# Performance work log

Measured on AMD Instinct MI355X. Metric: run time of the kernel, lower is better.

## Reference

```python
import jax, jax.numpy as jnp
import numpy as np

BLOCK = 64      # block_size
NRAND = 3       # num_random_blocks
NUM_HEAD = 16
HEAD_DIM = 64
HIDDEN = 1024
PEN = -10000.0  # HF attn_mask_penalty


def _sparse_attn(q, k, v, band_mask, from_mask, to_mask, blocked_mask, rand_attn):
    # q,k,v: [B,H,S,D]; BigBird block-sparse attention (HF math).
    B, H, S, D = q.shape
    b, r = BLOCK, NRAND
    n = S // b
    rsd = 1.0 / (D ** 0.5)

    bq = q.reshape(B, H, n, b, D)
    bk = k.reshape(B, H, n, b, D)
    bv = v.reshape(B, H, n, b, D)

    bi = jnp.arange(B)[:, None, None, None]
    hi = jnp.arange(H)[None, :, None, None]
    # gathered random key/value blocks: [B,H,n-2,r*b,D]
    gk = bk[bi, hi, rand_attn].reshape(B, H, n - 2, r * b, D)
    gv = bv[bi, hi, rand_attn].reshape(B, H, n - 2, r * b, D)
    # random-block mask: [B,H,n-2,b,r*b]
    rm = blocked_mask[bi, rand_attn].reshape(B, H, n - 2, r * b)
    rand_mask = jnp.einsum("blq,bhlk->bhlqk", blocked_mask[:, 1:-1], rm)

    ones = lambda shp: jnp.ones(shp, q.dtype)

    # ---- first query block: attends to everything ----
    p = jnp.einsum("bhqd,bhkd->bhqk", bq[:, :, 0], k) * rsd + (1.0 - to_mask) * PEN
    c0 = jnp.einsum("bhqk,bhkd->bhqd", jax.nn.softmax(p, -1), v)[:, :, None]

    # ---- second query block: blocks 0,1,2,last + random ----
    k1 = jnp.concatenate([bk[:, :, 0], bk[:, :, 1], bk[:, :, 2], bk[:, :, -1], gk[:, :, 0]], axis=2)
    v1 = jnp.concatenate([bv[:, :, 0], bv[:, :, 1], bv[:, :, 2], bv[:, :, -1], gv[:, :, 0]], axis=2)
    p = jnp.einsum("bhqd,bhkd->bhqk", bq[:, :, 1], k1) * rsd
    seq_pad = jnp.concatenate([to_mask[..., :3 * b], to_mask[..., -b:], ones((B, 1, 1, r * b))], axis=3)
    rand_pad = jnp.concatenate([ones((B, H, b, 4 * b)), rand_mask[:, :, 0]], axis=3)
    p = p + (1.0 - jnp.minimum(seq_pad, rand_pad)) * PEN
    c1 = jnp.einsum("bhqk,bhkd->bhqd", jax.nn.softmax(p, -1), v1)[:, :, None]

    # ---- middle blocks 2..n-3: band(3 blocks) + first + last + random ----
    ek = jnp.concatenate([bk[:, :, 1:-3], bk[:, :, 2:-2], bk[:, :, 3:-1]], axis=3)  # [B,H,n-4,3b,D]
    ev = jnp.concatenate([bv[:, :, 1:-3], bv[:, :, 2:-2], bv[:, :, 3:-1]], axis=3)
    mq = bq[:, :, 2:-2]                                                              # [B,H,n-4,b,D]
    inner = jnp.einsum("bhlqd,bhlkd->bhlqk", mq, ek) * rsd + (1.0 - band_mask) * PEN
    randp = jnp.einsum("bhlqd,bhlkd->bhlqk", mq, gk[:, :, 1:-1]) * rsd + (1.0 - rand_mask[:, :, 1:-1]) * PEN
    firstp = jnp.einsum("bhlqd,bhkd->bhlqk", mq, bk[:, :, 0]) * rsd + (1.0 - to_mask[..., :b][:, :, None]) * PEN
    lastp = jnp.einsum("bhlqd,bhkd->bhlqk", mq, bk[:, :, -1]) * rsd + (1.0 - to_mask[..., -b:][:, :, None]) * PEN
    band = jnp.concatenate([firstp, inner, randp, lastp], axis=-1)  # [B,H,n-4,b,(5+r)*b]
    a = jax.nn.softmax(band, -1)
    cm = jnp.einsum("bhlqk,bhlkd->bhlqd", a[..., b:4 * b], ev)
    cm = cm + jnp.einsum("bhlqk,bhlkd->bhlqd", a[..., 4 * b:-b], gv[:, :, 1:-1])
    cm = cm + jnp.einsum("bhlqk,bhkd->bhlqd", a[..., :b], bv[:, :, 0])
    cm = cm + jnp.einsum("bhlqk,bhkd->bhlqd", a[..., -b:], bv[:, :, -1])

    # ---- second-last query block: blocks 0,-3,-2,-1 + random ----
    k2 = jnp.concatenate([bk[:, :, 0], bk[:, :, -3], bk[:, :, -2], bk[:, :, -1], gk[:, :, -1]], axis=2)
    v2 = jnp.concatenate([bv[:, :, 0], bv[:, :, -3], bv[:, :, -2], bv[:, :, -1], gv[:, :, -1]], axis=2)
    p = jnp.einsum("bhqd,bhkd->bhqk", bq[:, :, -2], k2) * rsd
    seq_pad = jnp.concatenate([to_mask[..., :b], to_mask[..., -3 * b:], ones((B, 1, 1, r * b))], axis=3)
    rand_pad = jnp.concatenate([ones((B, H, b, 4 * b)), rand_mask[:, :, -1]], axis=3)
    p = p + (1.0 - jnp.minimum(seq_pad, rand_pad)) * PEN
    c2 = jnp.einsum("bhqk,bhkd->bhqd", jax.nn.softmax(p, -1), v2)[:, :, None]

    # ---- last query block: attends to everything ----
    p = jnp.einsum("bhqd,bhkd->bhqk", bq[:, :, -1], k) * rsd + (1.0 - to_mask) * PEN
    c3 = jnp.einsum("bhqk,bhkd->bhqd", jax.nn.softmax(p, -1), v)[:, :, None]

    ctx = jnp.concatenate([c0, c1, cm, c2, c3], axis=2).reshape(B, H, S, D)
    ctx = ctx * from_mask  # [B,1,S,1]
    return ctx.transpose(0, 2, 1, 3).reshape(B, S, H * D)


def setup_inputs() -> dict:
    key = jax.random.key(0)
    ks = jax.random.split(key, 12)
    B, L = 2, 4064
    S = 4096
    n = S // BLOCK
    sc = 0.02
    inp = {
        "X": jax.random.normal(ks[0], (B, L, HIDDEN), jnp.float32),
        "Wq": jax.random.normal(ks[1], (HIDDEN, NUM_HEAD * HEAD_DIM), jnp.float32) * sc,
        "b_q": jnp.zeros((NUM_HEAD * HEAD_DIM,), jnp.float32),
        "Wk": jax.random.normal(ks[2], (HIDDEN, NUM_HEAD * HEAD_DIM), jnp.float32) * sc,
        "b_k": jnp.zeros((NUM_HEAD * HEAD_DIM,), jnp.float32),
        "Wv": jax.random.normal(ks[3], (HIDDEN, NUM_HEAD * HEAD_DIM), jnp.float32) * sc,
        "b_v": jnp.zeros((NUM_HEAD * HEAD_DIM,), jnp.float32),
        "Wo": jax.random.normal(ks[4], (NUM_HEAD * HEAD_DIM, HIDDEN), jnp.float32) * sc,
        "b_o": jnp.zeros((HIDDEN,), jnp.float32),
        "band_mask": jnp.ones((B, 1, n - 4, BLOCK, 3 * BLOCK), jnp.float32),
        "from_mask": jnp.ones((B, 1, S, 1), jnp.float32),
        "to_mask": jnp.ones((B, 1, 1, S), jnp.float32),
        "blocked_encoder_mask": jnp.ones((B, n, BLOCK), jnp.float32),
        "rand_attn": jax.random.randint(ks[5], (B, NUM_HEAD, n - 2, NRAND), 0, n, jnp.int32),
    }
    return inp


def reference(X, Wq, b_q, Wk, b_k, Wv, b_v, Wo, b_o,
              band_mask, from_mask, to_mask, blocked_encoder_mask, rand_attn):
    B, L, _ = X.shape
    pad = BLOCK - L % BLOCK  # matches torch wrapper (pads full block if L % b == 0)
    Xp = jnp.pad(X, ((0, 0), (0, pad), (0, 0)))
    S = L + pad

    def proj(W, bias):
        return (Xp @ W + bias).reshape(B, S, NUM_HEAD, HEAD_DIM).transpose(0, 2, 1, 3)

    q, k, v = proj(Wq, b_q), proj(Wk, b_k), proj(Wv, b_v)
    attn = _sparse_attn(q, k, v, band_mask, from_mask, to_mask, blocked_encoder_mask, rand_attn)
    out = attn @ Wo + b_o
    return out[:, :L]
```

## Files before the change

kernel.cpp:

```cpp
#include <hip/hip_runtime.h>

#define BB 2
#define SEQ 4096
#define LQ 4064
#define HID 1024
#define NH 16
#define HD 64
#define NB 64
#define BLK 64
#define NR 3
#define PENV -10000.0f

typedef __bf16 bf16;
typedef __bf16 bf16x8 __attribute__((ext_vector_type(8)));
typedef float floatx4 __attribute__((ext_vector_type(4)));

__device__ inline floatx4 mfma16(bf16x8 a, bf16x8 b, floatx4 c) {
    return __builtin_amdgcn_mfma_f32_16x16x32_bf16(a, b, c, 0, 0, 0);
}

__device__ inline void async_ld16(const bf16* g, bf16* l) {
    __builtin_amdgcn_global_load_lds(
        (const __attribute__((address_space(1))) unsigned int*)g,
        (__attribute__((address_space(3))) unsigned int*)l, 16, 0, 0);
}

__global__ __launch_bounds__(256) void cast_pad_x(const float* __restrict__ X,
                                                  bf16* __restrict__ Xp) {
    int t = blockIdx.x * 256 + threadIdx.x;
    int c4 = t & 255;
    int row = t >> 8;
    int b = row >> 12;
    int s = row & 4095;
    float4 v = make_float4(0.f, 0.f, 0.f, 0.f);
    if (s < LQ) {
        v = reinterpret_cast<const float4*>(X + ((size_t)(b * LQ + s)) * HID)[c4];
    }
    union { bf16 h[4]; uint2 u; } o;
    o.h[0] = (bf16)v.x; o.h[1] = (bf16)v.y; o.h[2] = (bf16)v.z; o.h[3] = (bf16)v.w;
    *reinterpret_cast<uint2*>(Xp + (size_t)row * HID + c4 * 4) = o.u;
}

__global__ __launch_bounds__(256) void transpose_w(const float* __restrict__ Wq,
                                                   const float* __restrict__ Wk,
                                                   const float* __restrict__ Wv,
                                                   const float* __restrict__ Wo,
                                                   bf16* __restrict__ WqkvT,
                                                   bf16* __restrict__ WoT) {
    __shared__ float tile[64][65];
    int sel = blockIdx.z;
    const float* src = (sel == 0) ? Wq : (sel == 1) ? Wk : (sel == 2) ? Wv : Wo;
    bf16* dst = (sel < 3) ? (WqkvT + (size_t)sel * HID * HID) : WoT;
    int j0 = blockIdx.x * 64, k0 = blockIdx.y * 64;
    int tx = threadIdx.x, ty = threadIdx.y;
    for (int i = 0; i < 16; i++) {
        int k = ty + i * 4;
        tile[k][tx] = src[(size_t)(k0 + k) * HID + j0 + tx];
    }
    __syncthreads();
    for (int i = 0; i < 16; i++) {
        int j = ty + i * 4;
        dst[(size_t)(j0 + j) * HID + k0 + tx] = (bf16)tile[tx][j];
    }
}

__global__ __launch_bounds__(256) void transpose_band(const float* __restrict__ band,
                                                      float* __restrict__ bandT) {
    __shared__ float tile[64][65];
    int kt = blockIdx.x;
    int lrow = blockIdx.y;
    int b = blockIdx.z;
    const float* src = band + ((size_t)(b * (NB - 4) + lrow) * BLK) * 192;
    float* dst = bandT + ((size_t)(b * (NB - 4) + lrow) * 192) * BLK;
    int tx = threadIdx.x, ty = threadIdx.y;
    for (int i = 0; i < 16; i++) {
        int qq = i * 4 + ty;
        tile[qq][tx] = src[(size_t)qq * 192 + kt * 64 + tx];
    }
    __syncthreads();
    for (int i = 0; i < 16; i++) {
        int k = i * 4 + ty;
        dst[(size_t)(kt * 64 + k) * BLK + tx] = tile[tx][k];
    }
}

__global__ __launch_bounds__(256) void mask_viol(const float* __restrict__ tom,
                                                 const float* __restrict__ blocked,
                                                 const float* __restrict__ band,
                                                 int* __restrict__ flags) {
    int which = blockIdx.y, b = blockIdx.z;
    const float* src;
    size_t n;
    if (which == 0)      { src = tom     + (size_t)b * SEQ;                  n = SEQ; }
    else if (which == 1) { src = blocked + (size_t)b * NB * BLK;             n = NB * BLK; }
    else                 { src = band    + (size_t)b * (NB - 4) * BLK * 192; n = (size_t)(NB - 4) * BLK * 192; }
    const float4* s4 = (const float4*)src;
    size_t n4 = n >> 2;
    int bad = 0;
    for (size_t i = blockIdx.x * 256 + threadIdx.x; i < n4; i += 240 * 256) {
        float4 v = s4[i];
        bad |= (v.x != 1.0f) | (v.y != 1.0f) | (v.z != 1.0f) | (v.w != 1.0f);
    }
    if (__any(bad) && (threadIdx.x & 63) == 0)
        atomicOr(&flags[which * BB + b], 1);
}

__global__ __launch_bounds__(256) void gemm_qkv(const bf16* __restrict__ Xp,
                                                const bf16* __restrict__ WT,
                                                const float* __restrict__ bq,
                                                const float* __restrict__ bk,
                                                const float* __restrict__ bv,
                                                bf16* __restrict__ qo,
                                                bf16* __restrict__ ko,
                                                bf16* __restrict__ vt) {
    __shared__ __align__(16) char smem[36864];
    bf16* As = (bf16*)smem;
    bf16* Bs = As + 128 * 64;
    int tid = threadIdx.x;
    int wave = tid >> 6, lane = tid & 63;
    int quad = lane >> 4, lm = lane & 15;
    int id = blockIdx.x;
    int xcd = id & 7, slot = id >> 3;
    int tile_m = (xcd * 8 + (slot & 7)) * 128;
    int tile_n = (slot >> 3) * 128;
    int wm = (wave & 1) * 64, wn = (wave >> 1) * 64;

    floatx4 acc[4][4] = {};

    for (int k0 = 0; k0 < HID; k0 += 64) {
        __syncthreads();
        for (int it = 0; it < 4; it++) {
            int c = it * 256 + tid;
            int row = c >> 3, col = (c & 7) * 8;
            async_ld16(Xp + (size_t)(tile_m + row) * HID + k0 + col, &As[c * 8]);
            async_ld16(WT + (size_t)(tile_n + row) * HID + k0 + col, &Bs[c * 8]);
        }
        __syncthreads();
        for (int ks = 0; ks < 64; ks += 32) {
            bf16x8 a[4], b[4];
            for (int i = 0; i < 4; i++)
                a[i] = *reinterpret_cast<const bf16x8*>(&As[(wm + i * 16 + lm) * 64 + ks + quad * 8]);
            for (int j = 0; j < 4; j++)
                b[j] = *reinterpret_cast<const bf16x8*>(&Bs[(wn + j * 16 + lm) * 64 + ks + quad * 8]);
            for (int i = 0; i < 4; i++)
                for (int j = 0; j < 4; j++)
                    acc[i][j] = mfma16(a[i], b[j], acc[i][j]);
        }
    }

    int which = tile_n >> 10;
    int hc_base = (tile_n + wn) & 1023;
    int h = hc_base >> 6;
    const float* bias = (which == 0) ? bq : (which == 1) ? bk : bv;
    __syncthreads();
    bf16* ep = (bf16*)smem + wave * (64 * 72);

    if (which < 2) {
        #pragma unroll
        for (int i = 0; i < 4; i++)
            #pragma unroll
            for (int j = 0; j < 4; j++) {
                float bsv = bias[hc_base + j * 16 + lm];
                #pragma unroll
                for (int r = 0; r < 4; r++) {
                    float val = acc[i][j][r] + bsv;
                    if (which == 0) val *= 0.125f;
                    ep[(i * 16 + quad * 4 + r) * 72 + j * 16 + lm] = (bf16)val;
                }
            }
        __builtin_amdgcn_wave_barrier();
        int s_glob = tile_m + wm + lane;
        int b_ = s_glob >> 12, s = s_glob & 4095;
        bf16* dstb = ((which == 0) ? qo : ko) + ((size_t)((b_ * NH + h) * SEQ + s)) * HD;
        #pragma unroll
        for (int c = 0; c < 8; c++)
            *reinterpret_cast<uint4*>(dstb + c * 8) =
                *reinterpret_cast<const uint4*>(ep + lane * 72 + c * 8);
    } else {
        #pragma unroll
        for (int i = 0; i < 4; i++)
            #pragma unroll
            for (int j = 0; j < 4; j++) {
                float bsv = bias[hc_base + j * 16 + lm];
                #pragma unroll
                for (int r = 0; r < 4; r++) {
                    float val = acc[i][j][r] + bsv;
                    ep[(j * 16 + lm) * 72 + i * 16 + quad * 4 + r] = (bf16)val;
                }
            }
        __builtin_amdgcn_wave_barrier();
        int s_base = tile_m + wm;
        int b_ = s_base >> 12, s0 = s_base & 4095;
        bf16* dstb = vt + ((size_t)((b_ * NH + h) * HD + lane)) * SEQ + s0;
        #pragma unroll
        for (int c = 0; c < 8; c++)
            *reinterpret_cast<uint4*>(dstb + c * 8) =
                *reinterpret_cast<const uint4*>(ep + lane * 72 + c * 8);
    }
}

__global__ __launch_bounds__(256, 2) void attn_kernel(const bf16* __restrict__ q,
                                                      const bf16* __restrict__ kk,
                                                      const bf16* __restrict__ vt,
                                                      const float* __restrict__ bandT,
                                                      const float* __restrict__ fromm,
                                                      const float* __restrict__ tom,
                                                      const float* __restrict__ blocked,
                                                      const int* __restrict__ rand_attn,
                                                      const int* __restrict__ flags,
                                                      bf16* __restrict__ attn) {
    __shared__ __align__(16) char smem[33792 + 512];

    int tid = threadIdx.x, wave = tid >> 6, lane = tid & 63;
    int quad = lane >> 4, lm = lane & 15;
    int bh = blockIdx.x;
    int b = bh >> 4, h = bh & 15;
    size_t bh_base = (size_t)bh * SEQ * HD;
    int x = blockIdx.y;
    bool fullmode = (x < 8);
    int l, sub;
    if (fullmode) { l = (x >> 2) ? (NB - 1) : 0; sub = x & 3; }
    else          { l = x - 7;                   sub = wave;  }

    bool do_to = flags[b] != 0;
    bool do_bl = flags[BB + b] != 0;
    bool do_bd = flags[2 * BB + b] != 0;

    bf16x8 aq0 = *reinterpret_cast<const bf16x8*>(
        q + bh_base + (size_t)(l * BLK + sub * 16 + lm) * HD + quad * 8);
    bf16x8 aq1 = *reinterpret_cast<const bf16x8*>(
        q + bh_base + (size_t)(l * BLK + sub * 16 + lm) * HD + 32 + quad * 8);

    floatx4 ctx[4] = {};
    float mrun = -1e30f, lrun = 0.f;
    float mq = blocked[((size_t)b * NB + l) * BLK + sub * 16 + lm];

    int blist[8], btype[8];
    if (!fullmode) {
        int base;
        if (l == 1) {
            blist[0] = 0; blist[1] = 1; blist[2] = 2; blist[3] = NB - 1;
            btype[0] = btype[1] = btype[2] = btype[3] = 0;
            base = 4;
        } else if (l == NB - 2) {
            blist[0] = 0; blist[1] = NB - 3; blist[2] = NB - 2; blist[3] = NB - 1;
            btype[0] = btype[1] = btype[2] = btype[3] = 0;
            base = 4;
        } else {
            blist[0] = 0;      btype[0] = 0;
            blist[1] = l - 1;  btype[1] = 1;
            blist[2] = l;      btype[2] = 2;
            blist[3] = l + 1;  btype[3] = 3;
            blist[4] = NB - 1; btype[4] = 0;
            base = 5;
        }
        const int* ra = rand_attn + ((size_t)(b * NH + h) * (NB - 2) + (l - 1)) * NR;
        for (int r = 0; r < NR; r++) { blist[base + r] = ra[r]; btype[base + r] = 4; }
        for (int i = base + NR; i < 8; i++) { blist[i] = 0; btype[i] = 5; }
    }

    bf16* pw = (bf16*)smem + wave * 16 * 264;

    int nch = fullmode ? 4 : 2;
    for (int ch = 0; ch < nch; ch++) {
        floatx4 sc[4][4];
        #pragma unroll
        for (int ib = 0; ib < 4; ib++) {
            int kb  = fullmode ? (wave * 16 + ch * 4 + ib) : blist[ch * 4 + ib];
            int typ = fullmode ? 0 : btype[ch * 4 + ib];
            const bf16* kbase = kk + bh_base + (size_t)kb * BLK * HD;
            #pragma unroll
            for (int f = 0; f < 4; f++) {
                bf16x8 a0 = *reinterpret_cast<const bf16x8*>(kbase + (f * 16 + lm) * HD + quad * 8);
                bf16x8 a1 = *reinterpret_cast<const bf16x8*>(kbase + (f * 16 + lm) * HD + 32 + quad * 8);
                floatx4 z = {0.f, 0.f, 0.f, 0.f};
                z = mfma16(a0, aq0, z);
                z = mfma16(a1, aq1, z);
                sc[ib][f] = z;
            }
            if (typ == 0) {
                if (do_to) {
                    #pragma unroll
                    for (int f = 0; f < 4; f++) {
                        float4 t4 = *reinterpret_cast<const float4*>(
                            tom + (size_t)b * SEQ + kb * BLK + f * 16 + quad * 4);
                        sc[ib][f][0] += (1.f - t4.x) * PENV;
                        sc[ib][f][1] += (1.f - t4.y) * PENV;
                        sc[ib][f][2] += (1.f - t4.z) * PENV;
                        sc[ib][f][3] += (1.f - t4.w) * PENV;
                    }
                }
            } else if (typ == 4) {
                if (do_bl) {
                    #pragma unroll
                    for (int f = 0; f < 4; f++) {
                        float4 t4 = *reinterpret_cast<const float4*>(
                            blocked + ((size_t)b * NB + kb) * BLK + f * 16 + quad * 4);
                        sc[ib][f][0] += (1.f - mq * t4.x) * PENV;
                        sc[ib][f][1] += (1.f - mq * t4.y) * PENV;
                        sc[ib][f][2] += (1.f - mq * t4.z) * PENV;
                        sc[ib][f][3] += (1.f - mq * t4.w) * PENV;
                    }
                }
            } else if (typ != 5) {
                if (do_bd) {
                    int t = typ - 1;
                    const float* bp = bandT + ((size_t)(b * (NB - 4) + (l - 2)) * 192 + t * 64) * BLK;
                    #pragma unroll
                    for (int f = 0; f < 4; f++)
                        #pragma unroll
                        for (int r = 0; r < 4; r++) {
                            float bm = bp[(size_t)(f * 16 + quad * 4 + r) * BLK + sub * 16 + lm];
                            sc[ib][f][r] += (1.f - bm) * PENV;
                        }
                }
            } else {
                #pragma unroll
                for (int f = 0; f < 4; f++)
                    #pragma unroll
                    for (int r = 0; r < 4; r++) sc[ib][f][r] += PENV;
            }
        }

        float mx = -1e30f;
        #pragma unroll
        for (int ib = 0; ib < 4; ib++)
            #pragma unroll
            for (int f = 0; f < 4; f++)
                #pragma unroll
                for (int r = 0; r < 4; r++) mx = fmaxf(mx, sc[ib][f][r]);
        mx = fmaxf(mx, __shfl_xor(mx, 16, 64));
        mx = fmaxf(mx, __shfl_xor(mx, 32, 64));
        float mnew = fmaxf(mrun, mx);
        float scale = __expf(mrun - mnew);
        lrun *= scale;
        #pragma unroll
        for (int dj = 0; dj < 4; dj++) ctx[dj] *= scale;
        mrun = mnew;

        __builtin_amdgcn_wave_barrier();
        float rs = 0.f;
        #pragma unroll
        for (int ib = 0; ib < 4; ib++)
            #pragma unroll
            for (int f = 0; f < 4; f++) {
                float p0 = __expf(sc[ib][f][0] - mnew);
                float p1 = __expf(sc[ib][f][1] - mnew);
                float p2 = __expf(sc[ib][f][2] - mnew);
                float p3 = __expf(sc[ib][f][3] - mnew);
                rs += (p0 + p1) + (p2 + p3);
                union { bf16 hh[4]; uint2 u; } pu;
                pu.hh[0] = (bf16)p0; pu.hh[1] = (bf16)p1;
                pu.hh[2] = (bf16)p2; pu.hh[3] = (bf16)p3;
                *reinterpret_cast<uint2*>(pw + lm * 264 + ib * 64 + f * 16 + quad * 4) = pu.u;
            }
        __builtin_amdgcn_wave_barrier();
        rs += __shfl_xor(rs, 16, 64);
        rs += __shfl_xor(rs, 32, 64);
        lrun += rs;

        #pragma unroll
        for (int ib = 0; ib < 4; ib++) {
            int kb = fullmode ? (wave * 16 + ch * 4 + ib) : blist[ch * 4 + ib];
            const bf16* vtb = vt + (size_t)bh * HD * SEQ + (size_t)kb * BLK;
            bf16x8 pb0 = *reinterpret_cast<const bf16x8*>(pw + lm * 264 + ib * 64 + quad * 8);
            bf16x8 pb1 = *reinterpret_cast<const bf16x8*>(pw + lm * 264 + ib * 64 + 32 + quad * 8);
            #pragma unroll
            for (int dj = 0; dj < 4; dj++) {
                bf16x8 aV0 = *reinterpret_cast<const bf16x8*>(
                    vtb + (size_t)(dj * 16 + lm) * SEQ + quad * 8);
                bf16x8 aV1 = *reinterpret_cast<const bf16x8*>(
                    vtb + (size_t)(dj * 16 + lm) * SEQ + 32 + quad * 8);
                ctx[dj] = mfma16(aV0, pb0, ctx[dj]);
                ctx[dj] = mfma16(aV1, pb1, ctx[dj]);
            }
        }
    }

    if (!fullmode) {
        int sq = l * BLK + sub * 16 + lm;
        float w = (1.f / lrun) * fromm[(size_t)b * SEQ + sq];
        bf16* dst = attn + ((size_t)(b * SEQ + sq)) * HID + h * HD;
        #pragma unroll
        for (int dj = 0; dj < 4; dj++) {
            union { bf16 hh[4]; uint2 u; } o;
            #pragma unroll
            for (int r = 0; r < 4; r++) o.hh[r] = (bf16)(ctx[dj][r] * w);
            *reinterpret_cast<uint2*>(dst + dj * 16 + quad * 4) = o.u;
        }
    } else {
        float* ctxL = (float*)smem;
        float* mL   = (float*)(smem + 33792);
        float* lL   = (float*)(smem + 33792 + 256);
        __syncthreads();
        #pragma unroll
        for (int dj = 0; dj < 4; dj++)
            #pragma unroll
            for (int r = 0; r < 4; r++)
                ctxL[wave * 1024 + (dj * 16 + quad * 4 + r) * 16 + lm] = ctx[dj][r];
        if (quad == 0) { mL[wave * 16 + lm] = mrun; lL[wave * 16 + lm] = lrun; }
        __syncthreads();
        int qq = tid & 15, dbase = (tid >> 4) * 4;
        float M = -1e30f;
        for (int w = 0; w < 4; w++) M = fmaxf(M, mL[w * 16 + qq]);
        float e[4], Lt = 0.f;
        for (int w = 0; w < 4; w++) { e[w] = __expf(mL[w * 16 + qq] - M); Lt += lL[w * 16 + qq] * e[w]; }
        int sq = l * BLK + sub * 16 + qq;
        float wgt = (1.f / Lt) * fromm[(size_t)b * SEQ + sq];
        union { bf16 hh[4]; uint2 u; } o;
        #pragma unroll
        for (int dd = 0; dd < 4; dd++) {
            float acc = 0.f;
            for (int w = 0; w < 4; w++) acc += ctxL[w * 1024 + (dbase + dd) * 16 + qq] * e[w];
            o.hh[dd] = (bf16)(acc * wgt);
        }
        *reinterpret_cast<uint2*>(attn + ((size_t)(b * SEQ + sq)) * HID + h * HD + dbase) = o.u;
    }
}

__global__ __launch_bounds__(256) void gemm_out(const bf16* __restrict__ A,
                                                const bf16* __restrict__ WoT,
                                                const float* __restrict__ bo,
                                                float* __restrict__ out) {
    __shared__ __align__(16) bf16 As[128 * 64];
    __shared__ __align__(16) bf16 Bs[128 * 64];
    int tid = threadIdx.x;
    int wave = tid >> 6, lane = tid & 63;
    int quad = lane >> 4, lm = lane & 15;
    int id = blockIdx.x;
    int xcd = id & 7, slot = id >> 3;
    int tile_m = (xcd * 8 + (slot & 7)) * 128;
    int tile_n = (slot >> 3) * 128;
    int wm = (wave & 1) * 64, wn = (wave >> 1) * 64;

    floatx4 acc[4][4] = {};

    for (int k0 = 0; k0 < HID; k0 += 64) {
        __syncthreads();
        for (int it = 0; it < 4; it++) {
            int c = it * 256 + tid;
            int row = c >> 3, col = (c & 7) * 8;
            async_ld16(A + (size_t)(tile_m + row) * HID + k0 + col, &As[c * 8]);
            async_ld16(WoT + (size_t)(tile_n + row) * HID + k0 + col, &Bs[c * 8]);
        }
        __syncthreads();
        for (int ks = 0; ks < 64; ks += 32) {
            bf16x8 a[4], b[4];
            for (int i = 0; i < 4; i++)
                a[i] = *reinterpret_cast<const bf16x8*>(&As[(wm + i * 16 + lm) * 64 + ks + quad * 8]);
            for (int j = 0; j < 4; j++)
                b[j] = *reinterpret_cast<const bf16x8*>(&Bs[(wn + j * 16 + lm) * 64 + ks + quad * 8]);
            for (int i = 0; i < 4; i++)
                for (int j = 0; j < 4; j++)
                    acc[i][j] = mfma16(a[i], b[j], acc[i][j]);
        }
    }

    for (int i = 0; i < 4; i++) {
        for (int j = 0; j < 4; j++) {
            int nn = tile_n + wn + j * 16 + lm;
            float bsv = bo[nn];
            for (int r = 0; r < 4; r++) {
                int mm = tile_m + wm + i * 16 + quad * 4 + r;
                int b_ = mm >> 12, s = mm & 4095;
                if (s < LQ)
                    out[((size_t)(b_ * LQ + s)) * HID + nn] = acc[i][j][r] + bsv;
            }
        }
    }
}

extern "C" void kernel_launch(void* const* d_in, const int* in_sizes, int n_in,
                              void* d_out, int out_size, void* d_ws, size_t ws_size,
                              hipStream_t stream) {
    const float* X       = (const float*)d_in[0];
    const float* Wq      = (const float*)d_in[1];
    const float* bq      = (const float*)d_in[2];
    const float* Wk      = (const float*)d_in[3];
    const float* bk      = (const float*)d_in[4];
    const float* Wv      = (const float*)d_in[5];
    const float* bv      = (const float*)d_in[6];
    const float* Wo      = (const float*)d_in[7];
    const float* bo      = (const float*)d_in[8];
    const float* band    = (const float*)d_in[9];
    const float* fromm   = (const float*)d_in[10];
    const float* tom     = (const float*)d_in[11];
    const float* blocked = (const float*)d_in[12];
    const int*   randa   = (const int*)d_in[13];
    float* out = (float*)d_out;

    char* ws = (char*)d_ws;
    bf16* Xp    = (bf16*)(ws + 0);
    bf16* WqkvT = (bf16*)(ws + 16777216);
    bf16* WoT   = (bf16*)(ws + 23068672);
    bf16* qb    = (bf16*)(ws + 25165824);
    bf16* kb    = (bf16*)(ws + 41943040);
    bf16* vtb   = (bf16*)(ws + 58720256);
    bf16* attnb = Xp;
    float* bandT = (float*)WqkvT;
    int* flagsp = (int*)(ws + 16777216 + 5898240);

    cast_pad_x<<<dim3(8192), dim3(256), 0, stream>>>(X, Xp);
    transpose_w<<<dim3(16, 16, 4), dim3(64, 4), 0, stream>>>(Wq, Wk, Wv, Wo, WqkvT, WoT);
    gemm_qkv<<<dim3(1536), dim3(256), 0, stream>>>(Xp, WqkvT, bq, bk, bv, qb, kb, vtb);
    transpose_band<<<dim3(3, NB - 4, BB), dim3(64, 4), 0, stream>>>(band, bandT);
    hipMemsetAsync(flagsp, 0, 3 * BB * sizeof(int), stream);
    mask_viol<<<dim3(240, 3, BB), dim3(256), 0, stream>>>(tom, blocked, band, flagsp);
    attn_kernel<<<dim3(BB * NH, 70), dim3(256), 0, stream>>>(qb, kb, vtb, bandT, fromm, tom,
                                                             blocked, randa, flagsp, attnb);
    gemm_out<<<dim3(512), dim3(256), 0, stream>>>(attnb, WoT, bo, out);
}
```

Measured before the change: 392.1 us.

## Shrink attention chunk to two key blocks and raise occupancy to four blocks per CU

The attention kernel now handles two key blocks per softmax chunk instead of four. This halves the per-wave probability scratch in LDS and the score registers, which allows launch bounds of 4 blocks per CU. The block list and type arrays become packed 64-bit and 32-bit scalars, and block indices are made wave-uniform with readfirstlane. K fragments and the first V block are loaded ahead of the masking and softmax work so memory latency overlaps with compute. In exchange there are twice as many online-softmax rescale steps and wave barriers, and the tighter register budget could cause spills.

```diff
diff --git a/kernel.cpp b/kernel.cpp
--- a/kernel.cpp
+++ b/kernel.cpp
@@ -199,7 +199,7 @@
     }
 }
 
-__global__ __launch_bounds__(256, 2) void attn_kernel(const bf16* __restrict__ q,
+__global__ __launch_bounds__(256, 4) void attn_kernel(const bf16* __restrict__ q,
                                                       const bf16* __restrict__ kk,
                                                       const bf16* __restrict__ vt,
                                                       const float* __restrict__ bandT,
@@ -209,7 +209,7 @@
                                                       const int* __restrict__ rand_attn,
                                                       const int* __restrict__ flags,
                                                       bf16* __restrict__ attn) {
-    __shared__ __align__(16) char smem[33792 + 512];
+    __shared__ __align__(16) char smem[17408];
 
     int tid = threadIdx.x, wave = tid >> 6, lane = tid & 63;
     int quad = lane >> 4, lm = lane & 15;
@@ -235,100 +235,141 @@
     float mrun = -1e30f, lrun = 0.f;
     float mq = blocked[((size_t)b * NB + l) * BLK + sub * 16 + lm];
 
-    int blist[8], btype[8];
+    unsigned long long kbp = 0ull;
+    unsigned int typ_p = 0u;
     if (!fullmode) {
         int base;
         if (l == 1) {
-            blist[0] = 0; blist[1] = 1; blist[2] = 2; blist[3] = NB - 1;
-            btype[0] = btype[1] = btype[2] = btype[3] = 0;
+            kbp = (1ull << 8) | (2ull << 16) | ((unsigned long long)(NB - 1) << 24);
             base = 4;
         } else if (l == NB - 2) {
-            blist[0] = 0; blist[1] = NB - 3; blist[2] = NB - 2; blist[3] = NB - 1;
-            btype[0] = btype[1] = btype[2] = btype[3] = 0;
+            kbp = ((unsigned long long)(NB - 3) << 8) | ((unsigned long long)(NB - 2) << 16) |
+                  ((unsigned long long)(NB - 1) << 24);
             base = 4;
         } else {
-            blist[0] = 0;      btype[0] = 0;
-            blist[1] = l - 1;  btype[1] = 1;
-            blist[2] = l;      btype[2] = 2;
-            blist[3] = l + 1;  btype[3] = 3;
-            blist[4] = NB - 1; btype[4] = 0;
+            kbp = ((unsigned long long)(l - 1) << 8) | ((unsigned long long)l << 16) |
+                  ((unsigned long long)(l + 1) << 24) | ((unsigned long long)(NB - 1) << 32);
+            typ_p = (1u << 4) | (2u << 8) | (3u << 12);
             base = 5;
         }
         const int* ra = rand_attn + ((size_t)(b * NH + h) * (NB - 2) + (l - 1)) * NR;
-        for (int r = 0; r < NR; r++) { blist[base + r] = ra[r]; btype[base + r] = 4; }
-        for (int i = base + NR; i < 8; i++) { blist[i] = 0; btype[i] = 5; }
-    }
-
-    bf16* pw = (bf16*)smem + wave * 16 * 264;
-
-    int nch = fullmode ? 4 : 2;
+        #pragma unroll
+        for (int r = 0; r < NR; r++) {
+            int rv = __builtin_amdgcn_readfirstlane(ra[r]);
+            kbp   |= (unsigned long long)(rv & 63) << ((base + r) * 8);
+            typ_p |= 4u << ((base + r) * 4);
+        }
+        for (int i = base + NR; i < 8; i++) typ_p |= 5u << (i * 4);
+    }
+
+    bf16* pw = (bf16*)smem + wave * 16 * 136;
+
+    int nch = fullmode ? 8 : 4;
     for (int ch = 0; ch < nch; ch++) {
-        floatx4 sc[4][4];
-        #pragma unroll
-        for (int ib = 0; ib < 4; ib++) {
-            int kb  = fullmode ? (wave * 16 + ch * 4 + ib) : blist[ch * 4 + ib];
-            int typ = fullmode ? 0 : btype[ch * 4 + ib];
-            const bf16* kbase = kk + bh_base + (size_t)kb * BLK * HD;
+        int i0 = ch * 2, i1 = i0 + 1;
+        int kb0, kb1, ty0, ty1;
+        if (fullmode) {
+            kb0 = __builtin_amdgcn_readfirstlane(wave * 16 + i0);
+            kb1 = kb0 + 1;
+            ty0 = 0; ty1 = 0;
+        } else {
+            kb0 = __builtin_amdgcn_readfirstlane((int)((kbp >> (i0 * 8)) & 63));
+            kb1 = __builtin_amdgcn_readfirstlane((int)((kbp >> (i1 * 8)) & 63));
+            ty0 = (int)((typ_p >> (i0 * 4)) & 15);
+            ty1 = (int)((typ_p >> (i1 * 4)) & 15);
+        }
+
+        const bf16* k0p = kk + bh_base + (size_t)kb0 * (BLK * HD);
+        const bf16* k1p = kk + bh_base + (size_t)kb1 * (BLK * HD);
+        bf16x8 kfa[2][4], kfb[2][4];
+        #pragma unroll
+        for (int f = 0; f < 4; f++) {
+            kfa[0][f] = *reinterpret_cast<const bf16x8*>(k0p + (f * 16 + lm) * HD + quad * 8);
+            kfb[0][f] = *reinterpret_cast<const bf16x8*>(k0p + (f * 16 + lm) * HD + 32 + quad * 8);
+        }
+        #pragma unroll
+        for (int f = 0; f < 4; f++) {
+            kfa[1][f] = *reinterpret_cast<const bf16x8*>(k1p + (f * 16 + lm) * HD + quad * 8);
+            kfb[1][f] = *reinterpret_cast<const bf16x8*>(k1p + (f * 16 + lm) * HD + 32 + quad * 8);
+        }
+
+        floatx4 sc[2][4];
+        #pragma unroll
+        for (int u = 0; u < 2; u++)
             #pragma unroll
             for (int f = 0; f < 4; f++) {
-                bf16x8 a0 = *reinterpret_cast<const bf16x8*>(kbase + (f * 16 + lm) * HD + quad * 8);
-                bf16x8 a1 = *reinterpret_cast<const bf16x8*>(kbase + (f * 16 + lm) * HD + 32 + quad * 8);
                 floatx4 z = {0.f, 0.f, 0.f, 0.f};
-                z = mfma16(a0, aq0, z);
-                z = mfma16(a1, aq1, z);
-                sc[ib][f] = z;
+                z = mfma16(kfa[u][f], aq0, z);
+                z = mfma16(kfb[u][f], aq1, z);
+                sc[u][f] = z;
             }
-            if (typ == 0) {
-                if (do_to) {
-                    #pragma unroll
-                    for (int f = 0; f < 4; f++) {
-                        float4 t4 = *reinterpret_cast<const float4*>(
-                            tom + (size_t)b * SEQ + kb * BLK + f * 16 + quad * 4);
-                        sc[ib][f][0] += (1.f - t4.x) * PENV;
-                        sc[ib][f][1] += (1.f - t4.y) * PENV;
-                        sc[ib][f][2] += (1.f - t4.z) * PENV;
-                        sc[ib][f][3] += (1.f - t4.w) * PENV;
+
+        const bf16* v0p = vt + bh_base + (size_t)kb0 * BLK;
+        bf16x8 vf0[4][2];
+        #pragma unroll
+        for (int dj = 0; dj < 4; dj++) {
+            vf0[dj][0] = *reinterpret_cast<const bf16x8*>(v0p + (size_t)(dj * 16 + lm) * SEQ + quad * 8);
+            vf0[dj][1] = *reinterpret_cast<const bf16x8*>(v0p + (size_t)(dj * 16 + lm) * SEQ + 32 + quad * 8);
+        }
+
+        {
+            int kbs[2] = {kb0, kb1};
+            int tys[2] = {ty0, ty1};
+            #pragma unroll
+            for (int u = 0; u < 2; u++) {
+                int kb = kbs[u], typ = tys[u];
+                if (typ == 0) {
+                    if (do_to) {
+                        #pragma unroll
+                        for (int f = 0; f < 4; f++) {
+                            float4 t4 = *reinterpret_cast<const float4*>(
+                                tom + (size_t)b * SEQ + kb * BLK + f * 16 + quad * 4);
+                            sc[u][f][0] += (1.f - t4.x) * PENV;
+                            sc[u][f][1] += (1.f - t4.y) * PENV;
+                            sc[u][f][2] += (1.f - t4.z) * PENV;
+                            sc[u][f][3] += (1.f - t4.w) * PENV;
+                        }
                     }
-                }
-            } else if (typ == 4) {
-                if (do_bl) {
-                    #pragma unroll
-                    for (int f = 0; f < 4; f++) {
-                        float4 t4 = *reinterpret_cast<const float4*>(
-                            blocked + ((size_t)b * NB + kb) * BLK + f * 16 + quad * 4);
-                        sc[ib][f][0] += (1.f - mq * t4.x) * PENV;
-                        sc[ib][f][1] += (1.f - mq * t4.y) * PENV;
-                        sc[ib][f][2] += (1.f - mq * t4.z) * PENV;
-                        sc[ib][f][3] += (1.f - mq * t4.w) * PENV;
+                } else if (typ == 4) {
+                    if (do_bl) {
+                        #pragma unroll
+                        for (int f = 0; f < 4; f++) {
+                            float4 t4 = *reinterpret_cast<const float4*>(
+                                blocked + ((size_t)b * NB + kb) * BLK + f * 16 + quad * 4);
+                            sc[u][f][0] += (1.f - mq * t4.x) * PENV;
+                            sc[u][f][1] += (1.f - mq * t4.y) * PENV;
+                            sc[u][f][2] += (1.f - mq * t4.z) * PENV;
+                            sc[u][f][3] += (1.f - mq * t4.w) * PENV;
+                        }
                     }
-                }
-            } else if (typ != 5) {
-                if (do_bd) {
-                    int t = typ - 1;
-                    const float* bp = bandT + ((size_t)(b * (NB - 4) + (l - 2)) * 192 + t * 64) * BLK;
+                } else if (typ != 5) {
+                    if (do_bd) {
+                        int t = typ - 1;
+                        const float* bp = bandT + ((size_t)(b * (NB - 4) + (l - 2)) * 192 + t * 64) * BLK;
+                        #pragma unroll
+                        for (int f = 0; f < 4; f++)
+                            #pragma unroll
+                            for (int r = 0; r < 4; r++) {
+                                float bm = bp[(size_t)(f * 16 + quad * 4 + r) * BLK + sub * 16 + lm];
+                                sc[u][f][r] += (1.f - bm) * PENV;
+                            }
+                    }
+                } else {
                     #pragma unroll
                     for (int f = 0; f < 4; f++)
                         #pragma unroll
-                        for (int r = 0; r < 4; r++) {
-                            float bm = bp[(size_t)(f * 16 + quad * 4 + r) * BLK + sub * 16 + lm];
-                            sc[ib][f][r] += (1.f - bm) * PENV;
-                        }
+                        for (int r = 0; r < 4; r++) sc[u][f][r] += PENV;
                 }
-            } else {
-                #pragma unroll
-                for (int f = 0; f < 4; f++)
-                    #pragma unroll
-                    for (int r = 0; r < 4; r++) sc[ib][f][r] += PENV;
             }
         }
 
         float mx = -1e30f;
         #pragma unroll
-        for (int ib = 0; ib < 4; ib++)
+        for (int u = 0; u < 2; u++)
             #pragma unroll
             for (int f = 0; f < 4; f++)
                 #pragma unroll
-                for (int r = 0; r < 4; r++) mx = fmaxf(mx, sc[ib][f][r]);
+                for (int r = 0; r < 4; r++) mx = fmaxf(mx, sc[u][f][r]);
         mx = fmaxf(mx, __shfl_xor(mx, 16, 64));
         mx = fmaxf(mx, __shfl_xor(mx, 32, 64));
         float mnew = fmaxf(mrun, mx);
@@ -341,39 +382,47 @@
         __builtin_amdgcn_wave_barrier();
         float rs = 0.f;
         #pragma unroll
-        for (int ib = 0; ib < 4; ib++)
+        for (int u = 0; u < 2; u++)
             #pragma unroll
             for (int f = 0; f < 4; f++) {
-                float p0 = __expf(sc[ib][f][0] - mnew);
-                float p1 = __expf(sc[ib][f][1] - mnew);
-                float p2 = __expf(sc[ib][f][2] - mnew);
-                float p3 = __expf(sc[ib][f][3] - mnew);
+                float p0 = __expf(sc[u][f][0] - mnew);
+                float p1 = __expf(sc[u][f][1] - mnew);
+                float p2 = __expf(sc[u][f][2] - mnew);
+                float p3 = __expf(sc[u][f][3] - mnew);
                 rs += (p0 + p1) + (p2 + p3);
-                union { bf16 hh[4]; uint2 u; } pu;
+                union { bf16 hh[4]; uint2 u2; } pu;
                 pu.hh[0] = (bf16)p0; pu.hh[1] = (bf16)p1;
                 pu.hh[2] = (bf16)p2; pu.hh[3] = (bf16)p3;
-                *reinterpret_cast<uint2*>(pw + lm * 264 + ib * 64 + f * 16 + quad * 4) = pu.u;
+                *reinterpret_cast<uint2*>(pw + lm * 136 + u * 64 + f * 16 + quad * 4) = pu.u2;
             }
         __builtin_amdgcn_wave_barrier();
         rs += __shfl_xor(rs, 16, 64);
         rs += __shfl_xor(rs, 32, 64);
         lrun += rs;
 
-        #pragma unroll
-        for (int ib = 0; ib < 4; ib++) {
-            int kb = fullmode ? (wave * 16 + ch * 4 + ib) : blist[ch * 4 + ib];
-            const bf16* vtb = vt + (size_t)bh * HD * SEQ + (size_t)kb * BLK;
-            bf16x8 pb0 = *reinterpret_cast<const bf16x8*>(pw + lm * 264 + ib * 64 + quad * 8);
-            bf16x8 pb1 = *reinterpret_cast<const bf16x8*>(pw + lm * 264 + ib * 64 + 32 + quad * 8);
-            #pragma unroll
-            for (int dj = 0; dj < 4; dj++) {
-                bf16x8 aV0 = *reinterpret_cast<const bf16x8*>(
-                    vtb + (size_t)(dj * 16 + lm) * SEQ + quad * 8);
-                bf16x8 aV1 = *reinterpret_cast<const bf16x8*>(
-                    vtb + (size_t)(dj * 16 + lm) * SEQ + 32 + quad * 8);
-                ctx[dj] = mfma16(aV0, pb0, ctx[dj]);
-                ctx[dj] = mfma16(aV1, pb1, ctx[dj]);
-            }
+        bf16x8 pb[2][2];
+        #pragma unroll
+        for (int u = 0; u < 2; u++) {
+            pb[u][0] = *reinterpret_cast<const bf16x8*>(pw + lm * 136 + u * 64 + quad * 8);
+            pb[u][1] = *reinterpret_cast<const bf16x8*>(pw + lm * 136 + u * 64 + 32 + quad * 8);
+        }
+
+        #pragma unroll
+        for (int dj = 0; dj < 4; dj++) {
+            ctx[dj] = mfma16(vf0[dj][0], pb[0][0], ctx[dj]);
+            ctx[dj] = mfma16(vf0[dj][1], pb[0][1], ctx[dj]);
+        }
+        const bf16* v1p = vt + bh_base + (size_t)kb1 * BLK;
+        bf16x8 vf1[4][2];
+        #pragma unroll
+        for (int dj = 0; dj < 4; dj++) {
+            vf1[dj][0] = *reinterpret_cast<const bf16x8*>(v1p + (size_t)(dj * 16 + lm) * SEQ + quad * 8);
+            vf1[dj][1] = *reinterpret_cast<const bf16x8*>(v1p + (size_t)(dj * 16 + lm) * SEQ + 32 + quad * 8);
+        }
+        #pragma unroll
+        for (int dj = 0; dj < 4; dj++) {
+            ctx[dj] = mfma16(vf1[dj][0], pb[1][0], ctx[dj]);
+            ctx[dj] = mfma16(vf1[dj][1], pb[1][1], ctx[dj]);
         }
     }
 
@@ -383,15 +432,15 @@
         bf16* dst = attn + ((size_t)(b * SEQ + sq)) * HID + h * HD;
         #pragma unroll
         for (int dj = 0; dj < 4; dj++) {
-            union { bf16 hh[4]; uint2 u; } o;
+            union { bf16 hh[4]; uint2 u2; } o;
             #pragma unroll
             for (int r = 0; r < 4; r++) o.hh[r] = (bf16)(ctx[dj][r] * w);
-            *reinterpret_cast<uint2*>(dst + dj * 16 + quad * 4) = o.u;
+            *reinterpret_cast<uint2*>(dst + dj * 16 + quad * 4) = o.u2;
         }
     } else {
         float* ctxL = (float*)smem;
-        float* mL   = (float*)(smem + 33792);
-        float* lL   = (float*)(smem + 33792 + 256);
+        float* mL   = (float*)(smem + 16384);
+        float* lL   = (float*)(smem + 16640);
         __syncthreads();
         #pragma unroll
         for (int dj = 0; dj < 4; dj++)
@@ -407,14 +456,14 @@
         for (int w = 0; w < 4; w++) { e[w] = __expf(mL[w * 16 + qq] - M); Lt += lL[w * 16 + qq] * e[w]; }
         int sq = l * BLK + sub * 16 + qq;
         float wgt = (1.f / Lt) * fromm[(size_t)b * SEQ + sq];
-        union { bf16 hh[4]; uint2 u; } o;
+        union { bf16 hh[4]; uint2 u2; } o;
         #pragma unroll
         for (int dd = 0; dd < 4; dd++) {
             float acc = 0.f;
             for (int w = 0; w < 4; w++) acc += ctxL[w * 1024 + (dbase + dd) * 16 + qq] * e[w];
             o.hh[dd] = (bf16)(acc * wgt);
         }
-        *reinterpret_cast<uint2*>(attn + ((size_t)(b * SEQ + sq)) * HID + h * HD + dbase) = o.u;
+        *reinterpret_cast<uint2*>(attn + ((size_t)(b * SEQ + sq)) * HID + h * HD + dbase) = o.u2;
     }
 }
 
```

New measurement: 409.2 us. 4.4% more time.
